# Kernel optimization log

Measured on AMD Instinct MI355X. Metric: run time of the kernel, lower is better.

Reference implementation:

```python
import jax, jax.numpy as jnp
import numpy as np

N_NODES = 50000
N_EDGES = 150000
N_TRIS = 100000
F = 256
L = 4


def setup_inputs() -> dict:
    key = jax.random.key(0)
    ks = jax.random.split(key, 8)
    x = jax.random.normal(ks[0], (N_EDGES, F), dtype=jnp.float32)
    edge_nodes = jax.random.randint(ks[1], (N_EDGES, 2), 0, N_NODES)
    tri_edges = jax.random.randint(ks[2], (N_TRIS, 3), 0, N_EDGES)
    tri_signs = (jax.random.randint(ks[3], (N_TRIS, 3), 0, 2) * 2 - 1).astype(jnp.int32)
    std = float(np.sqrt(2.0 / (F + F)))  # xavier_uniform-equivalent std
    W0_stack = jax.random.normal(ks[4], (L, F, F), dtype=jnp.float32) * std
    W1_stack = jax.random.normal(ks[5], (L, F, F), dtype=jnp.float32) * std
    W2_stack = jax.random.normal(ks[6], (L, F, F), dtype=jnp.float32) * std
    W0_L = jax.random.normal(ks[7], (F, 1), dtype=jnp.float32) * float(np.sqrt(2.0 / (F + 1)))
    return {"x": x, "W0_stack": W0_stack, "W1_stack": W1_stack, "W2_stack": W2_stack,
            "W0_L": W0_L, "edge_nodes": edge_nodes, "tri_edges": tri_edges, "tri_signs": tri_signs}


def _b1_mm(edge_nodes, y):
    # B1 @ y : [E,F] -> [N,F];  B1[u,e] = -1, B1[v,e] = +1
    u, v = edge_nodes[:, 0], edge_nodes[:, 1]
    out = jnp.zeros((N_NODES, y.shape[1]), y.dtype)
    return out.at[u].add(-y).at[v].add(y)


def _b1t_mm(edge_nodes, z):
    # B1.T @ z : [N,F] -> [E,F]
    return z[edge_nodes[:, 1]] - z[edge_nodes[:, 0]]


def _b2t_mm(tri_edges, signs, y):
    # B2.T @ y : [E,F] -> [T,F]
    return jnp.einsum('tkf,tk->tf', y[tri_edges], signs)


def _b2_mm(tri_edges, signs, w):
    # B2 @ w : [T,F] -> [E,F]
    contrib = w[:, None, :] * signs[:, :, None]  # [T,3,F]
    out = jnp.zeros((N_EDGES, w.shape[1]), w.dtype)
    return out.at[tri_edges.reshape(-1)].add(contrib.reshape(-1, w.shape[1]))


def reference(x, W0_stack, W1_stack, W2_stack, W0_L, edge_nodes, tri_edges, tri_signs):
    signs = tri_signs.astype(x.dtype)
    for i in range(L):
        d2 = _b2_mm(tri_edges, signs, _b2t_mm(tri_edges, signs, x @ W2_stack[i]))
        d1 = x @ W1_stack[i]
        d0 = _b1t_mm(edge_nodes, _b1_mm(edge_nodes, x @ W0_stack[i]))
        x = jax.nn.relu(d2 + d1 + d0)
    return _b1_mm(edge_nodes, x @ W0_L)  # [N_NODES, 1]
```

## Files before the change

### kernel.cpp

```cpp
#include <hip/hip_runtime.h>

#define M_EDGES 150000
#define NN_NODES 50000
#define N_TRIS  100000
#define F 256
#define NLAYERS 4

#define T0 1172
#define T1 391
#define T2 782
#define T0_PAD 1176
#define G0_BLOCKS (T0_PAD * 2)
#define T12 (T1 + T2)
#define T12_PAD 1176
#define G12_BLOCKS (T12_PAD * 2)

#define ZN_BLOCKS (NN_NODES / 4)
#define WT_BLOCKS (N_TRIS / 4)

typedef __attribute__((ext_vector_type(8))) __bf16 bf16x8;
typedef __attribute__((ext_vector_type(4))) float f32x4;

__device__ inline unsigned short f2bf(float f) {
    unsigned int u = __float_as_uint(f);
    u += 0x7fff + ((u >> 16) & 1);
    return (unsigned short)(u >> 16);
}
__device__ inline float bf2f(unsigned short h) {
    return __uint_as_float(((unsigned int)h) << 16);
}

__device__ inline void async16(const void* g, void* l) {
    __builtin_amdgcn_global_load_lds(
        (const __attribute__((address_space(1))) void*)g,
        (__attribute__((address_space(3))) void*)l, 16, 0, 0);
}

__device__ inline void gemm_kloop(
    const unsigned short* __restrict__ Asrc, int nrows,
    const unsigned short* __restrict__ wseg,
    int bm0, int bn,
    unsigned short* As, unsigned short* Bs,
    f32x4 cacc[4][4])
{
    const int tid  = threadIdx.x;
    const int wid  = tid >> 6;
    const int lane = tid & 63;
    const int lm   = lane & 15;
    const int lh   = lane >> 4;
    const int wm   = wid >> 1;
    const int wn   = wid & 1;
    const int wbase = tid & ~63;

    for (int k0 = 0; k0 < 256; k0 += 32) {
#pragma unroll
        for (int s = 0; s < 2; s++) {
            int i   = s * 256 + tid;
            int row = i >> 2;
            int g   = (i & 3) ^ ((row >> 1) & 3);
            int gr  = bm0 + row;
            if (gr > nrows - 1) gr = nrows - 1;
            async16(Asrc + (size_t)gr * 256 + k0 + g * 8,
                    As + (size_t)(s * 256 + wbase) * 8);
            int nrow = bn * 128 + row;
            async16(wseg + (size_t)nrow * 256 + k0 + g * 8,
                    Bs + (size_t)(s * 256 + wbase) * 8);
        }
        asm volatile("s_waitcnt vmcnt(0)" ::: "memory");
        __syncthreads();

        bf16x8 a[4], bfr[4];
#pragma unroll
        for (int i = 0; i < 4; i++) {
            int rr = wm * 64 + i * 16 + lm;
            a[i] = *(const bf16x8*)(As + rr * 32 + ((lh ^ ((rr >> 1) & 3)) * 8));
        }
#pragma unroll
        for (int j = 0; j < 4; j++) {
            int rr = wn * 64 + j * 16 + lm;
            bfr[j] = *(const bf16x8*)(Bs + rr * 32 + ((lh ^ ((rr >> 1) & 3)) * 8));
        }
#pragma unroll
        for (int i = 0; i < 4; i++)
#pragma unroll
            for (int j = 0; j < 4; j++)
                cacc[i][j] = __builtin_amdgcn_mfma_f32_16x16x32_bf16(bfr[j], a[i], cacc[i][j], 0, 0, 0);
        __syncthreads();
    }
}

__global__ __launch_bounds__(256) void gemm12(
    const unsigned short* __restrict__ sb,
    const unsigned short* __restrict__ qb,
    const unsigned short* __restrict__ wt,
    unsigned short* __restrict__ zb,
    unsigned short* __restrict__ wb)
{
    __shared__ unsigned short As[128 * 32];
    __shared__ unsigned short Bs[128 * 32];

    const int b    = blockIdx.x;
    const int xcd  = b & 7;
    const int c    = b >> 3;
    const int tile = (c >> 1) * 8 + xcd;
    const int bn   = c & 1;
    if (tile >= T12) return;

    const unsigned short* Asrc;
    const unsigned short* wseg;
    unsigned short* dst;
    int nrows, tloc;
    if (tile < T1) { Asrc = sb; wseg = wt + 65536;  dst = zb; nrows = NN_NODES; tloc = tile; }
    else           { Asrc = qb; wseg = wt + 131072; dst = wb; nrows = N_TRIS;   tloc = tile - T1; }

    f32x4 cacc[4][4];
#pragma unroll
    for (int i = 0; i < 4; i++)
#pragma unroll
        for (int j = 0; j < 4; j++) cacc[i][j] = (f32x4){0.f, 0.f, 0.f, 0.f};

    const int bm0 = tloc * 128;
    gemm_kloop(Asrc, nrows, wseg, bm0, bn, As, Bs, cacc);

    const int tid  = threadIdx.x;
    const int lane = tid & 63;
    const int lm   = lane & 15;
    const int lh   = lane >> 4;
    const int wm   = (tid >> 6) >> 1;
    const int wn   = (tid >> 6) & 1;
#pragma unroll
    for (int i = 0; i < 4; i++) {
        int grow = bm0 + wm * 64 + i * 16 + lm;
        if (grow < nrows) {
#pragma unroll
            for (int j = 0; j < 4; j++) {
                int col = bn * 128 + wn * 64 + j * 16 + lh * 4;
                ushort4 r;
                r.x = f2bf(cacc[i][j][0]);
                r.y = f2bf(cacc[i][j][1]);
                r.z = f2bf(cacc[i][j][2]);
                r.w = f2bf(cacc[i][j][3]);
                *(ushort4*)(dst + (size_t)grow * 256 + col) = r;
            }
        }
    }
}

__global__ __launch_bounds__(256) void gemm0_relu(
    const unsigned short* __restrict__ xin,
    const unsigned short* __restrict__ wt,
    const unsigned short* __restrict__ zb,
    const unsigned short* __restrict__ wb,
    const int* __restrict__ en,
    const int* __restrict__ eoff,
    const int* __restrict__ eadj,
    unsigned short* __restrict__ xout)
{
    __shared__ unsigned short As[128 * 32];
    __shared__ unsigned short Bs[128 * 32];

    const int b    = blockIdx.x;
    const int xcd  = b & 7;
    const int c    = b >> 3;
    const int tile = (c >> 1) * 8 + xcd;
    const int bn   = c & 1;
    if (tile >= T0) return;

    f32x4 cacc[4][4];
#pragma unroll
    for (int i = 0; i < 4; i++)
#pragma unroll
        for (int j = 0; j < 4; j++) cacc[i][j] = (f32x4){0.f, 0.f, 0.f, 0.f};

    const int bm0 = tile * 128;
    gemm_kloop(xin, M_EDGES, wt, bm0, bn, As, Bs, cacc);

    const int tid  = threadIdx.x;
    const int lane = tid & 63;
    const int lm   = lane & 15;
    const int lh   = lane >> 4;
    const int wm   = (tid >> 6) >> 1;
    const int wn   = (tid >> 6) & 1;
    const int colb = bn * 128 + wn * 64 + lh * 4;

#pragma unroll
    for (int i = 0; i < 4; i++) {
        int e = bm0 + wm * 64 + i * 16 + lm;
        if (e < M_EDGES) {
            int u = en[2 * e], v = en[2 * e + 1];
            int beg = eoff[e], end = eoff[e + 1];
            float s0[4], s1[4], s2[4], s3[4];
#pragma unroll
            for (int j = 0; j < 4; j++) {
                int col = colb + j * 16;
                ushort4 zvv = *(const ushort4*)(zb + (size_t)v * 256 + col);
                ushort4 zuu = *(const ushort4*)(zb + (size_t)u * 256 + col);
                s0[j] = cacc[i][j][0] + bf2f(zvv.x) - bf2f(zuu.x);
                s1[j] = cacc[i][j][1] + bf2f(zvv.y) - bf2f(zuu.y);
                s2[j] = cacc[i][j][2] + bf2f(zvv.z) - bf2f(zuu.z);
                s3[j] = cacc[i][j][3] + bf2f(zvv.w) - bf2f(zuu.w);
            }
            for (int it = beg; it < end; it++) {
                int ent = eadj[it];
                float sg = (ent & 1) ? -1.f : 1.f;
                const unsigned short* wr = wb + (size_t)(ent >> 1) * 256;
#pragma unroll
                for (int j = 0; j < 4; j++) {
                    int col = colb + j * 16;
                    ushort4 wv = *(const ushort4*)(wr + col);
                    s0[j] += sg * bf2f(wv.x);
                    s1[j] += sg * bf2f(wv.y);
                    s2[j] += sg * bf2f(wv.z);
                    s3[j] += sg * bf2f(wv.w);
                }
            }
#pragma unroll
            for (int j = 0; j < 4; j++) {
                int col = colb + j * 16;
                ushort4 r;
                r.x = f2bf(fmaxf(s0[j], 0.f));
                r.y = f2bf(fmaxf(s1[j], 0.f));
                r.z = f2bf(fmaxf(s2[j], 0.f));
                r.w = f2bf(fmaxf(s3[j], 0.f));
                *(ushort4*)(xout + (size_t)e * 256 + col) = r;
            }
        }
    }
}

__global__ __launch_bounds__(256) void count_nodes(
    const int* __restrict__ en, int* __restrict__ cnt)
{
    int e = blockIdx.x * 256 + threadIdx.x;
    if (e < M_EDGES) {
        atomicAdd(&cnt[en[2 * e]], 1);
        atomicAdd(&cnt[en[2 * e + 1]], 1);
    }
}

__global__ __launch_bounds__(256) void count_tris(
    const int* __restrict__ te, int* __restrict__ cnt)
{
    int t = blockIdx.x * 256 + threadIdx.x;
    if (t < N_TRIS) {
#pragma unroll
        for (int k = 0; k < 3; k++) atomicAdd(&cnt[te[3 * t + k]], 1);
    }
}

__global__ __launch_bounds__(256) void scan_block(
    const int* __restrict__ cnt, int* __restrict__ off,
    int* __restrict__ partial, int n)
{
    __shared__ int s[256];
    int t = threadIdx.x;
    int gid = blockIdx.x * 256 + t;
    int v = (gid < n) ? cnt[gid] : 0;
    s[t] = v;
    __syncthreads();
    for (int o = 1; o < 256; o <<= 1) {
        int x = (t >= o) ? s[t - o] : 0;
        __syncthreads();
        s[t] += x;
        __syncthreads();
    }
    if (gid < n) off[gid] = s[t] - v;
    if (t == 255) partial[blockIdx.x] = s[255];
}

__global__ __launch_bounds__(1024) void scan_partial(int* __restrict__ partial, int nb)
{
    __shared__ int s[1024];
    int t = threadIdx.x;
    int v = (t < nb) ? partial[t] : 0;
    s[t] = v;
    __syncthreads();
    for (int o = 1; o < 1024; o <<= 1) {
        int x = (t >= o) ? s[t - o] : 0;
        __syncthreads();
        s[t] += x;
        __syncthreads();
    }
    if (t < nb) partial[t] = s[t] - v;
}

__global__ __launch_bounds__(256) void scan_add(
    int* __restrict__ off, int* __restrict__ cursor,
    const int* __restrict__ partial, int n, int total)
{
    int gid = blockIdx.x * 256 + threadIdx.x;
    if (gid == 0) off[n] = total;
    if (gid < n) {
        int o = off[gid] + partial[blockIdx.x];
        off[gid] = o;
        cursor[gid] = o;
    }
}

__global__ __launch_bounds__(256) void fill_nodes(
    const int* __restrict__ en, int* __restrict__ cursor, int* __restrict__ adj)
{
    int e = blockIdx.x * 256 + threadIdx.x;
    if (e < M_EDGES) {
        int u = en[2 * e], v = en[2 * e + 1];
        adj[atomicAdd(&cursor[u], 1)] = (e << 1);
        adj[atomicAdd(&cursor[v], 1)] = (e << 1) | 1;
    }
}

__global__ __launch_bounds__(256) void fill_tris(
    const int* __restrict__ te, const int* __restrict__ ts,
    int* __restrict__ cursor, int* __restrict__ adj)
{
    int t = blockIdx.x * 256 + threadIdx.x;
    if (t < N_TRIS) {
#pragma unroll
        for (int k = 0; k < 3; k++) {
            int e = te[3 * t + k];
            int neg = (ts[3 * t + k] < 0) ? 1 : 0;
            adj[atomicAdd(&cursor[e], 1)] = (t << 1) | neg;
        }
    }
}

__global__ __launch_bounds__(256) void agg_fused(
    const unsigned short* __restrict__ xb,
    const int* __restrict__ noff,
    const int* __restrict__ nadj,
    unsigned short* __restrict__ sbuf,
    const int* __restrict__ te,
    const int* __restrict__ ts,
    unsigned short* __restrict__ qbuf)
{
    int lane = threadIdx.x & 63;
    int f = lane * 4;
    if (blockIdx.x < ZN_BLOCKS) {
        int n = blockIdx.x * 4 + (threadIdx.x >> 6);
        int beg = noff[n], end = noff[n + 1];
        float ax = 0.f, ay = 0.f, az = 0.f, aw = 0.f;
        int i = beg;
        for (; i + 1 < end; i += 2) {
            int ea = nadj[i], eb = nadj[i + 1];
            float sa = (ea & 1) ? 1.f : -1.f;
            float sgb = (eb & 1) ? 1.f : -1.f;
            ushort4 va = *(const ushort4*)(xb + (size_t)(ea >> 1) * 256 + f);
            ushort4 vb = *(const ushort4*)(xb + (size_t)(eb >> 1) * 256 + f);
            ax += sa * bf2f(va.x) + sgb * bf2f(vb.x);
            ay += sa * bf2f(va.y) + sgb * bf2f(vb.y);
            az += sa * bf2f(va.z) + sgb * bf2f(vb.z);
            aw += sa * bf2f(va.w) + sgb * bf2f(vb.w);
        }
        if (i < end) {
            int ea = nadj[i];
            float sa = (ea & 1) ? 1.f : -1.f;
            ushort4 va = *(const ushort4*)(xb + (size_t)(ea >> 1) * 256 + f);
            ax += sa * bf2f(va.x);
            ay += sa * bf2f(va.y);
            az += sa * bf2f(va.z);
            aw += sa * bf2f(va.w);
        }
        ushort4 r;
        r.x = f2bf(ax); r.y = f2bf(ay); r.z = f2bf(az); r.w = f2bf(aw);
        *(ushort4*)(sbuf + (size_t)n * 256 + f) = r;
    } else {
        int t = (blockIdx.x - ZN_BLOCKS) * 4 + (threadIdx.x >> 6);
        int e0 = te[3 * t + 0], e1 = te[3 * t + 1], e2 = te[3 * t + 2];
        float s0 = (float)ts[3 * t + 0];
        float s1 = (float)ts[3 * t + 1];
        float s2 = (float)ts[3 * t + 2];
        ushort4 a4 = *(const ushort4*)(xb + (size_t)e0 * 256 + f);
        ushort4 b4 = *(const ushort4*)(xb + (size_t)e1 * 256 + f);
        ushort4 d4 = *(const ushort4*)(xb + (size_t)e2 * 256 + f);
        ushort4 r;
        r.x = f2bf(s0 * bf2f(a4.x) + s1 * bf2f(b4.x) + s2 * bf2f(d4.x));
        r.y = f2bf(s0 * bf2f(a4.y) + s1 * bf2f(b4.y) + s2 * bf2f(d4.y));
        r.z = f2bf(s0 * bf2f(a4.z) + s1 * bf2f(b4.z) + s2 * bf2f(d4.z));
        r.w = f2bf(s0 * bf2f(a4.w) + s1 * bf2f(b4.w) + s2 * bf2f(d4.w));
        *(ushort4*)(qbuf + (size_t)t * 256 + f) = r;
    }
}

__global__ __launch_bounds__(256) void dotp(
    const unsigned short* __restrict__ xb,
    const float* __restrict__ wl,
    float* __restrict__ p)
{
    int e = blockIdx.x * 4 + (threadIdx.x >> 6);
    int lane = threadIdx.x & 63;
    ushort4 xv = *(const ushort4*)(xb + (size_t)e * 256 + lane * 4);
    float4 wv = *(const float4*)(wl + lane * 4);
    float s = bf2f(xv.x) * wv.x + bf2f(xv.y) * wv.y +
              bf2f(xv.z) * wv.z + bf2f(xv.w) * wv.w;
#pragma unroll
    for (int off = 32; off > 0; off >>= 1)
        s += __shfl_down(s, off, 64);
    if (lane == 0) p[e] = s;
}

__global__ __launch_bounds__(256) void out_nodes(
    const float* __restrict__ p,
    const int* __restrict__ noff,
    const int* __restrict__ nadj,
    float* __restrict__ out)
{
    int n = blockIdx.x * 256 + threadIdx.x;
    if (n >= NN_NODES) return;
    int beg = noff[n], end = noff[n + 1];
    float s = 0.f;
    for (int i = beg; i < end; i++) {
        int ent = nadj[i];
        float sg = (ent & 1) ? 1.f : -1.f;
        s += sg * p[ent >> 1];
    }
    out[n] = s;
}

__global__ __launch_bounds__(256) void cvt_x(
    const float* __restrict__ x, unsigned short* __restrict__ xb)
{
    int idx = blockIdx.x * 256 + threadIdx.x;
    float4 v = *(const float4*)(x + (size_t)idx * 4);
    ushort4 r;
    r.x = f2bf(v.x); r.y = f2bf(v.y); r.z = f2bf(v.z); r.w = f2bf(v.w);
    *(ushort4*)(xb + (size_t)idx * 4) = r;
}

__global__ __launch_bounds__(256) void cvt_w(
    const float* __restrict__ W0, const float* __restrict__ W1,
    const float* __restrict__ W2, unsigned short* __restrict__ wt)
{
    int idx = blockIdx.x * 256 + threadIdx.x;
    int l = idx / (3 * 65536);
    int rem = idx - l * (3 * 65536);
    int seg = rem >> 16;
    int n = (rem >> 8) & 255;
    int k = rem & 255;
    const float* src = (seg == 0) ? W1 : (seg == 1) ? W0 : W2;
    wt[idx] = f2bf(src[(size_t)l * 65536 + k * 256 + n]);
}

extern "C" void kernel_launch(void* const* d_in, const int* in_sizes, int n_in,
                              void* d_out, int out_size, void* d_ws, size_t ws_size,
                              hipStream_t stream)
{
    const float* x0  = (const float*)d_in[0];
    const float* W0s = (const float*)d_in[1];
    const float* W1s = (const float*)d_in[2];
    const float* W2s = (const float*)d_in[3];
    const float* WL  = (const float*)d_in[4];
    const int*   en  = (const int*)d_in[5];
    const int*   te  = (const int*)d_in[6];
    const int*   ts  = (const int*)d_in[7];
    float* out = (float*)d_out;

    const size_t MF = (size_t)M_EDGES * F;
    unsigned short* xb  = (unsigned short*)d_ws;
    unsigned short* xb2 = xb + MF;
    unsigned short* sbuf = xb2 + MF;
    unsigned short* qbuf = sbuf + (size_t)NN_NODES * 256;
    unsigned short* wt = qbuf + (size_t)N_TRIS * 256;
    unsigned short* wb = wt + (size_t)4 * 3 * 65536;
    unsigned short* zb = wb + (size_t)N_TRIS * 256;
    float* p = (float*)(zb + (size_t)NN_NODES * 256);
    int* noff = (int*)(p + M_EDGES);
    int* ncur = noff + (NN_NODES + 1);
    int* nadj = ncur + NN_NODES;
    int* eoff = nadj + 2 * M_EDGES;
    int* ecur = eoff + (M_EDGES + 1);
    int* eadj = ecur + M_EDGES;
    int* part = eadj + 3 * N_TRIS;

    cvt_w<<<(4 * 3 * 65536) / 256, 256, 0, stream>>>(W0s, W1s, W2s, wt);
    cvt_x<<<(int)(MF / 4 / 256), 256, 0, stream>>>(x0, xb);

    const int nbN = (NN_NODES + 255) / 256;
    const int nbE = (M_EDGES + 255) / 256;
    hipMemsetAsync(ncur, 0, NN_NODES * sizeof(int), stream);
    hipMemsetAsync(ecur, 0, M_EDGES * sizeof(int), stream);
    count_nodes<<<nbE, 256, 0, stream>>>(en, ncur);
    count_tris<<<(N_TRIS + 255) / 256, 256, 0, stream>>>(te, ecur);
    scan_block<<<nbN, 256, 0, stream>>>(ncur, noff, part, NN_NODES);
    scan_partial<<<1, 1024, 0, stream>>>(part, nbN);
    scan_add<<<nbN, 256, 0, stream>>>(noff, ncur, part, NN_NODES, 2 * M_EDGES);
    fill_nodes<<<nbE, 256, 0, stream>>>(en, ncur, nadj);
    scan_block<<<nbE, 256, 0, stream>>>(ecur, eoff, part, M_EDGES);
    scan_partial<<<1, 1024, 0, stream>>>(part, nbE);
    scan_add<<<nbE, 256, 0, stream>>>(eoff, ecur, part, M_EDGES, 3 * N_TRIS);
    fill_tris<<<(N_TRIS + 255) / 256, 256, 0, stream>>>(te, ts, ecur, eadj);

    for (int l = 0; l < NLAYERS; l++) {
        const unsigned short* wl_ = wt + (size_t)l * 3 * 65536;
        const unsigned short* xin = (l & 1) ? xb2 : xb;
        unsigned short* xout      = (l & 1) ? xb : xb2;
        agg_fused<<<ZN_BLOCKS + WT_BLOCKS, 256, 0, stream>>>(
            xin, noff, nadj, sbuf, te, ts, qbuf);
        gemm12<<<G12_BLOCKS, 256, 0, stream>>>(sbuf, qbuf, wl_, zb, wb);
        gemm0_relu<<<G0_BLOCKS, 256, 0, stream>>>(
            xin, wl_, zb, wb, en, eoff, eadj, xout);
    }

    dotp<<<M_EDGES / 4, 256, 0, stream>>>(xb, WL, p);
    out_nodes<<<(NN_NODES + 255) / 256, 256, 0, stream>>>(p, noff, nadj, out);
}
```

Before: 1.360 ms.

## Stage GEMM tile in LDS and do row-wise coalesced gather epilogue

The fused gemm0_relu epilogue now writes the bf16 GEMM accumulators into a padded shared-memory tile. Each wave then processes whole edge rows, with lanes spanning contiguous columns, for the node-difference and triangle-adjacency gathers. Previously each lane handled a different edge, so gathers were scattered and the variable-length adjacency loop diverged within a wave. The trade-offs are a larger LDS footprint, which may reduce occupancy, and rounding the GEMM result to bf16 before the additions.

```diff
diff --git a/kernel.cpp b/kernel.cpp
--- a/kernel.cpp
+++ b/kernel.cpp
@@ -17,6 +17,8 @@
 
 #define ZN_BLOCKS (NN_NODES / 4)
 #define WT_BLOCKS (N_TRIS / 4)
+
+#define LDSROW 136
 
 typedef __attribute__((ext_vector_type(8))) __bf16 bf16x8;
 typedef __attribute__((ext_vector_type(4))) float f32x4;
@@ -156,8 +158,9 @@
     const int* __restrict__ eadj,
     unsigned short* __restrict__ xout)
 {
-    __shared__ unsigned short As[128 * 32];
-    __shared__ unsigned short Bs[128 * 32];
+    __shared__ unsigned short smem[128 * LDSROW];
+    unsigned short* As = smem;
+    unsigned short* Bs = smem + 128 * 32;
 
     const int b    = blockIdx.x;
     const int xcd  = b & 7;
@@ -176,55 +179,54 @@
     gemm_kloop(xin, M_EDGES, wt, bm0, bn, As, Bs, cacc);
 
     const int tid  = threadIdx.x;
+    const int wid  = tid >> 6;
     const int lane = tid & 63;
     const int lm   = lane & 15;
     const int lh   = lane >> 4;
-    const int wm   = (tid >> 6) >> 1;
-    const int wn   = (tid >> 6) & 1;
-    const int colb = bn * 128 + wn * 64 + lh * 4;
+    const int wm   = wid >> 1;
+    const int wn   = wid & 1;
 
 #pragma unroll
     for (int i = 0; i < 4; i++) {
-        int e = bm0 + wm * 64 + i * 16 + lm;
-        if (e < M_EDGES) {
-            int u = en[2 * e], v = en[2 * e + 1];
-            int beg = eoff[e], end = eoff[e + 1];
-            float s0[4], s1[4], s2[4], s3[4];
-#pragma unroll
-            for (int j = 0; j < 4; j++) {
-                int col = colb + j * 16;
-                ushort4 zvv = *(const ushort4*)(zb + (size_t)v * 256 + col);
-                ushort4 zuu = *(const ushort4*)(zb + (size_t)u * 256 + col);
-                s0[j] = cacc[i][j][0] + bf2f(zvv.x) - bf2f(zuu.x);
-                s1[j] = cacc[i][j][1] + bf2f(zvv.y) - bf2f(zuu.y);
-                s2[j] = cacc[i][j][2] + bf2f(zvv.z) - bf2f(zuu.z);
-                s3[j] = cacc[i][j][3] + bf2f(zvv.w) - bf2f(zuu.w);
-            }
-            for (int it = beg; it < end; it++) {
-                int ent = eadj[it];
-                float sg = (ent & 1) ? -1.f : 1.f;
-                const unsigned short* wr = wb + (size_t)(ent >> 1) * 256;
-#pragma unroll
-                for (int j = 0; j < 4; j++) {
-                    int col = colb + j * 16;
-                    ushort4 wv = *(const ushort4*)(wr + col);
-                    s0[j] += sg * bf2f(wv.x);
-                    s1[j] += sg * bf2f(wv.y);
-                    s2[j] += sg * bf2f(wv.z);
-                    s3[j] += sg * bf2f(wv.w);
-                }
-            }
-#pragma unroll
-            for (int j = 0; j < 4; j++) {
-                int col = colb + j * 16;
-                ushort4 r;
-                r.x = f2bf(fmaxf(s0[j], 0.f));
-                r.y = f2bf(fmaxf(s1[j], 0.f));
-                r.z = f2bf(fmaxf(s2[j], 0.f));
-                r.w = f2bf(fmaxf(s3[j], 0.f));
-                *(ushort4*)(xout + (size_t)e * 256 + col) = r;
-            }
-        }
+        int row = wm * 64 + i * 16 + lm;
+#pragma unroll
+        for (int j = 0; j < 4; j++) {
+            int col = wn * 64 + j * 16 + lh * 4;
+            ushort4 r;
+            r.x = f2bf(cacc[i][j][0]);
+            r.y = f2bf(cacc[i][j][1]);
+            r.z = f2bf(cacc[i][j][2]);
+            r.w = f2bf(cacc[i][j][3]);
+            *(ushort4*)(&smem[row * LDSROW + col]) = r;
+        }
+    }
+    __syncthreads();
+
+    const int colbase = bn * 128;
+    for (int r = 0; r < 32; r++) {
+        int row = wid * 32 + r;
+        int e = bm0 + row;
+        if (e >= M_EDGES) break;
+        ushort2 lv = *(ushort2*)(&smem[row * LDSROW + lane * 2]);
+        float sA = bf2f(lv.x), sB = bf2f(lv.y);
+        int u = en[2 * e], v = en[2 * e + 1];
+        int cc = colbase + lane * 2;
+        ushort2 zv2 = *(const ushort2*)(zb + (size_t)v * 256 + cc);
+        ushort2 zu2 = *(const ushort2*)(zb + (size_t)u * 256 + cc);
+        sA += bf2f(zv2.x) - bf2f(zu2.x);
+        sB += bf2f(zv2.y) - bf2f(zu2.y);
+        int beg = eoff[e], end = eoff[e + 1];
+        for (int it = beg; it < end; it++) {
+            int ent = eadj[it];
+            float sg = (ent & 1) ? -1.f : 1.f;
+            ushort2 wv = *(const ushort2*)(wb + (size_t)(ent >> 1) * 256 + cc);
+            sA += sg * bf2f(wv.x);
+            sB += sg * bf2f(wv.y);
+        }
+        ushort2 o;
+        o.x = f2bf(fmaxf(sA, 0.f));
+        o.y = f2bf(fmaxf(sB, 0.f));
+        *(ushort2*)(xout + (size_t)e * 256 + cc) = o;
     }
 }
 
```

New measurement: 1.799 ms. 1.32x slower.
